# Kernel tuning notes

Measured on AMD Instinct MI355X. Metric: run time of the kernel, lower is better.

The kernel has to match this reference:

```python
import jax, jax.numpy as jnp
import numpy as np

SCALE = 0.125  # 1/sqrt(d_k), d_k = 64


def setup_inputs() -> dict:
    key = jax.random.key(0)
    kq, kk, kv, kp = jax.random.split(key, 4)
    H, B, L, T, D = 16, 4, 1024, 1024, 64
    return {
        "query": jax.random.normal(kq, (H, B, L, D), dtype=jnp.float32),
        "key": jax.random.normal(kk, (H, B, T, D), dtype=jnp.float32),
        "value": jax.random.normal(kv, (H, B, T, D), dtype=jnp.float32),
        "prev_attention": jax.random.normal(kp, (H, B, L, T), dtype=jnp.float32),
    }


def reference(query, key, value, prev_attention):
    # scores: [h, b, l, t]
    scores = jnp.einsum("hblk,hbtk->hblt", query, key) * SCALE
    scores = scores + prev_attention
    attention = jax.nn.softmax(scores, axis=-1)
    # dropout disabled (rate 0.0) for deterministic reference
    output = jnp.einsum("hblt,hbtv->hblv", attention, value)
    return (output, attention)
```

## Files before the change

### kernel.cpp

```cpp
#include <hip/hip_runtime.h>

#define SCALE 0.125f

constexpr int L_ = 1024, T_ = 1024, D_ = 64, HB_ = 64;

using f32x4 = __attribute__((ext_vector_type(4))) float;
using half8 = __attribute__((ext_vector_type(8))) _Float16;
using half4 = __attribute__((ext_vector_type(4))) _Float16;

__global__ __launch_bounds__(256) void cvt_v(const float* __restrict__ v,
                                             _Float16* __restrict__ vh) {
  __shared__ _Float16 ts[64][136];
  const int tid = threadIdx.x;
  const int hb = blockIdx.y;
  const int t0 = blockIdx.x * 128;
  {
    const int tr = tid >> 1, dh = (tid & 1) * 32;
    const float* p = v + ((size_t)hb * T_ + t0 + tr) * D_ + dh;
#pragma unroll
    for (int i = 0; i < 8; ++i) {
      f32x4 r = *(const f32x4*)(p + i * 4);
#pragma unroll
      for (int e = 0; e < 4; ++e) ts[dh + i * 4 + e][tr] = (_Float16)r[e];
    }
  }
  __syncthreads();
  {
    const int d = tid >> 2, tq = (tid & 3) * 32;
    _Float16* qo = vh + ((size_t)hb * D_ + d) * T_ + t0 + tq;
#pragma unroll
    for (int i = 0; i < 4; ++i)
      *(half8*)(qo + i * 8) = *(const half8*)&ts[d][tq + i * 8];
  }
}

__global__ __launch_bounds__(512) void attn_all(
    const float* __restrict__ q, const float* __restrict__ kk,
    const _Float16* __restrict__ Vh, const float* __restrict__ prev,
    float* __restrict__ out, float* __restrict__ att) {
  __shared__ __align__(16) _Float16 Ks[1024][70];
  __shared__ __align__(16) _Float16 Pl[8][16][64];

  const int ltile = blockIdx.x;
  const int hb    = blockIdx.y;
  const int tid = threadIdx.x;
  const int w = tid >> 6, l = tid & 63, l15 = l & 15, lg = l >> 4;
  const int qrow = ltile * 128 + w * 16 + l15;

  auto plb = [&](int row, int byte) -> _Float16* {
    return (_Float16*)((unsigned char*)&Pl[w][0][0] + row * 128 +
                       ((unsigned)byte ^ (((unsigned)row & 7) << 4)));
  };

  {
    const int srow = tid >> 2, scol = (tid & 3) * 16;
    const float* kp0 = kk + (size_t)hb * T_ * D_;
#pragma unroll
    for (int rep = 0; rep < 8; ++rep) {
      const int r = rep * 128 + srow;
      const float* p = kp0 + (size_t)r * D_ + scol;
      f32x4 a = *(const f32x4*)(p);
      f32x4 b = *(const f32x4*)(p + 4);
      f32x4 cc = *(const f32x4*)(p + 8);
      f32x4 d = *(const f32x4*)(p + 12);
      half8 h0, h1;
#pragma unroll
      for (int e = 0; e < 4; ++e) {
        h0[e] = (_Float16)a[e];  h0[4 + e] = (_Float16)b[e];
        h1[e] = (_Float16)cc[e]; h1[4 + e] = (_Float16)d[e];
      }
      *(half8*)&Ks[r][scol] = h0;
      *(half8*)&Ks[r][scol + 8] = h1;
    }
  }

  half8 qb2[2];
  {
    const float* qp = q + ((size_t)hb * L_ + qrow) * D_ + lg * 8;
#pragma unroll
    for (int f = 0; f < 2; ++f)
#pragma unroll
      for (int e = 0; e < 8; ++e) qb2[f][e] = (_Float16)qp[f * 32 + e];
  }

  const float* prowb =
      prev + ((size_t)hb * L_ + ltile * 128 + w * 16) * (size_t)T_;
  const int cr = l >> 4, cc4 = (l & 15) * 4;

  f32x4 pr[2][4];
  auto pload = [&](int c, int s) {
#pragma unroll
    for (int i = 0; i < 4; ++i)
      pr[s][i] =
          *(const f32x4*)(prowb + (size_t)(cr + 4 * i) * T_ + c * 64 + cc4);
  };
  auto pstage = [&](int s) {
#pragma unroll
    for (int i = 0; i < 4; ++i) {
      half4 h;
      h[0] = (_Float16)pr[s][i][0]; h[1] = (_Float16)pr[s][i][1];
      h[2] = (_Float16)pr[s][i][2]; h[3] = (_Float16)pr[s][i][3];
      *(half4*)plb(cr + 4 * i, cc4 * 2) = h;
    }
  };

  __syncthreads();

  pload(0, 0);
  pload(1, 1);
  float zsum = 0.f;

#pragma unroll 2
  for (int c = 0; c < 16; ++c) {
    pstage(c & 1);
    if (c < 14) pload(c + 2, c & 1);

#pragma unroll
    for (int nt = 0; nt < 4; ++nt) {
      const int trow = c * 64 + nt * 16 + l15;
      half8 ka0 = *(const half8*)&Ks[trow][lg * 8];
      half8 ka1 = *(const half8*)&Ks[trow][32 + lg * 8];
      f32x4 acc = {0.f, 0.f, 0.f, 0.f};
      acc = __builtin_amdgcn_mfma_f32_16x16x32_f16(ka0, qb2[0], acc, 0, 0, 0);
      acc = __builtin_amdgcn_mfma_f32_16x16x32_f16(ka1, qb2[1], acc, 0, 0, 0);

      half4 hv = *(const half4*)plb(l15, (nt * 16 + lg * 4) * 2);
      zsum += __expf(acc[0] * SCALE + (float)hv[0]);
      zsum += __expf(acc[1] * SCALE + (float)hv[1]);
      zsum += __expf(acc[2] * SCALE + (float)hv[2]);
      zsum += __expf(acc[3] * SCALE + (float)hv[3]);
    }
  }

  zsum += __shfl_xor(zsum, 16, 64);
  zsum += __shfl_xor(zsum, 32, 64);
  const float rzq = 1.0f / zsum;

  const _Float16* vbh = Vh + (size_t)hb * D_ * T_;
  float* attb = att + ((size_t)hb * L_ + ltile * 128 + w * 16) * (size_t)T_;

  half8 vr[2][8];
  auto vload = [&](int c, int s) {
#pragma unroll
    for (int ks = 0; ks < 2; ++ks)
#pragma unroll
      for (int nd = 0; nd < 4; ++nd)
        vr[s][ks * 4 + nd] =
            *(const half8*)(vbh + (size_t)(nd * 16 + l15) * T_ + c * 64 +
                            ks * 32 + lg * 8);
  };

  pload(0, 0);
  pload(1, 1);
  vload(0, 0);
  vload(1, 1);

  f32x4 oacc[4];
#pragma unroll
  for (int nd = 0; nd < 4; ++nd) oacc[nd] = (f32x4){0.f, 0.f, 0.f, 0.f};

#pragma unroll 2
  for (int c = 0; c < 16; ++c) {
    pstage(c & 1);
    if (c < 14) pload(c + 2, c & 1);

#pragma unroll
    for (int nt = 0; nt < 4; ++nt) {
      const int trow = c * 64 + nt * 16 + l15;
      half8 ka0 = *(const half8*)&Ks[trow][lg * 8];
      half8 ka1 = *(const half8*)&Ks[trow][32 + lg * 8];
      f32x4 acc = {0.f, 0.f, 0.f, 0.f};
      acc = __builtin_amdgcn_mfma_f32_16x16x32_f16(ka0, qb2[0], acc, 0, 0, 0);
      acc = __builtin_amdgcn_mfma_f32_16x16x32_f16(ka1, qb2[1], acc, 0, 0, 0);

      half4 hv = *(const half4*)plb(l15, (nt * 16 + lg * 4) * 2);
      float s0 = __expf(acc[0] * SCALE + (float)hv[0]) * rzq;
      float s1 = __expf(acc[1] * SCALE + (float)hv[1]) * rzq;
      float s2 = __expf(acc[2] * SCALE + (float)hv[2]) * rzq;
      float s3 = __expf(acc[3] * SCALE + (float)hv[3]) * rzq;
      half4 sv;
      sv[0] = (_Float16)s0; sv[1] = (_Float16)s1;
      sv[2] = (_Float16)s2; sv[3] = (_Float16)s3;
      *(half4*)plb(l15, (nt * 16 + lg * 4) * 2) = sv;
    }

#pragma unroll
    for (int ks = 0; ks < 2; ++ks) {
      half8 af = *(const half8*)plb(l15, (ks * 32 + lg * 8) * 2);
#pragma unroll
      for (int nd = 0; nd < 4; ++nd)
        oacc[nd] = __builtin_amdgcn_mfma_f32_16x16x32_f16(
            af, vr[c & 1][ks * 4 + nd], oacc[nd], 0, 0, 0);
    }

#pragma unroll
    for (int i = 0; i < 4; ++i) {
      half4 hv = *(const half4*)plb(cr + 4 * i, cc4 * 2);
      f32x4 sv = {(float)hv[0], (float)hv[1], (float)hv[2], (float)hv[3]};
      *(f32x4*)(attb + (size_t)(cr + 4 * i) * T_ + c * 64 + cc4) = sv;
    }

    if (c < 14) vload(c + 2, c & 1);
  }

  float* outw =
      out + ((size_t)hb * L_ + ltile * 128 + w * 16 + lg * 4) * (size_t)D_;
#pragma unroll
  for (int nd = 0; nd < 4; ++nd)
#pragma unroll
    for (int i = 0; i < 4; ++i)
      outw[(size_t)i * D_ + nd * 16 + l15] = oacc[nd][i];
}

extern "C" void kernel_launch(void* const* d_in, const int* in_sizes, int n_in,
                              void* d_out, int out_size, void* d_ws,
                              size_t ws_size, hipStream_t stream) {
  const float* q    = (const float*)d_in[0];
  const float* k    = (const float*)d_in[1];
  const float* v    = (const float*)d_in[2];
  const float* prev = (const float*)d_in[3];

  float* out = (float*)d_out;
  float* att = out + (size_t)HB_ * L_ * D_;

  _Float16* Vh = (_Float16*)d_ws;

  cvt_v<<<dim3(T_ / 128, HB_), 256, 0, stream>>>(v, Vh);
  attn_all<<<dim3(L_ / 128, HB_), 512, 0, stream>>>(q, k, Vh, prev, out, att);
}
```

Measured before the change: 209.4 us.

## Cache unnormalized exponentials in registers to skip second pass recompute and prev reload

The first softmax pass now keeps every exp(score) as fp16 in a per-thread register array while it accumulates the row sum. The second pass just scales those cached values by the reciprocal sum, so it no longer reloads prev_attention from global memory or recomputes the QK^T MFMAs and exponentials. This cuts the dominant global read traffic roughly in half. In exchange it adds heavy register pressure (128 extra VGPRs, full loop unroll), which risks spills or lower occupancy, and it rounds exp values to fp16 before normalising.

```diff
diff --git a/kernel.cpp b/kernel.cpp
--- a/kernel.cpp
+++ b/kernel.cpp
@@ -106,11 +106,12 @@
 
   __syncthreads();
 
+  half4 E[16][4];
   pload(0, 0);
   pload(1, 1);
   float zsum = 0.f;
 
-#pragma unroll 2
+#pragma unroll
   for (int c = 0; c < 16; ++c) {
     pstage(c & 1);
     if (c < 14) pload(c + 2, c & 1);
@@ -125,16 +126,21 @@
       acc = __builtin_amdgcn_mfma_f32_16x16x32_f16(ka1, qb2[1], acc, 0, 0, 0);
 
       half4 hv = *(const half4*)plb(l15, (nt * 16 + lg * 4) * 2);
-      zsum += __expf(acc[0] * SCALE + (float)hv[0]);
-      zsum += __expf(acc[1] * SCALE + (float)hv[1]);
-      zsum += __expf(acc[2] * SCALE + (float)hv[2]);
-      zsum += __expf(acc[3] * SCALE + (float)hv[3]);
+      float e0 = __expf(acc[0] * SCALE + (float)hv[0]);
+      float e1 = __expf(acc[1] * SCALE + (float)hv[1]);
+      float e2 = __expf(acc[2] * SCALE + (float)hv[2]);
+      float e3 = __expf(acc[3] * SCALE + (float)hv[3]);
+      zsum += (e0 + e1) + (e2 + e3);
+      half4 ev;
+      ev[0] = (_Float16)e0; ev[1] = (_Float16)e1;
+      ev[2] = (_Float16)e2; ev[3] = (_Float16)e3;
+      E[c][nt] = ev;
     }
   }
 
   zsum += __shfl_xor(zsum, 16, 64);
   zsum += __shfl_xor(zsum, 32, 64);
-  const float rzq = 1.0f / zsum;
+  const _Float16 rzh = (_Float16)(1.0f / zsum);
 
   const _Float16* vbh = Vh + (size_t)hb * D_ * T_;
   float* attb = att + ((size_t)hb * L_ + ltile * 128 + w * 16) * (size_t)T_;
@@ -149,9 +155,6 @@
             *(const half8*)(vbh + (size_t)(nd * 16 + l15) * T_ + c * 64 +
                             ks * 32 + lg * 8);
   };
-
-  pload(0, 0);
-  pload(1, 1);
   vload(0, 0);
   vload(1, 1);
 
@@ -159,28 +162,14 @@
 #pragma unroll
   for (int nd = 0; nd < 4; ++nd) oacc[nd] = (f32x4){0.f, 0.f, 0.f, 0.f};
 
-#pragma unroll 2
+#pragma unroll
   for (int c = 0; c < 16; ++c) {
-    pstage(c & 1);
-    if (c < 14) pload(c + 2, c & 1);
-
 #pragma unroll
     for (int nt = 0; nt < 4; ++nt) {
-      const int trow = c * 64 + nt * 16 + l15;
-      half8 ka0 = *(const half8*)&Ks[trow][lg * 8];
-      half8 ka1 = *(const half8*)&Ks[trow][32 + lg * 8];
-      f32x4 acc = {0.f, 0.f, 0.f, 0.f};
-      acc = __builtin_amdgcn_mfma_f32_16x16x32_f16(ka0, qb2[0], acc, 0, 0, 0);
-      acc = __builtin_amdgcn_mfma_f32_16x16x32_f16(ka1, qb2[1], acc, 0, 0, 0);
-
-      half4 hv = *(const half4*)plb(l15, (nt * 16 + lg * 4) * 2);
-      float s0 = __expf(acc[0] * SCALE + (float)hv[0]) * rzq;
-      float s1 = __expf(acc[1] * SCALE + (float)hv[1]) * rzq;
-      float s2 = __expf(acc[2] * SCALE + (float)hv[2]) * rzq;
-      float s3 = __expf(acc[3] * SCALE + (float)hv[3]) * rzq;
+      half4 ev = E[c][nt];
       half4 sv;
-      sv[0] = (_Float16)s0; sv[1] = (_Float16)s1;
-      sv[2] = (_Float16)s2; sv[3] = (_Float16)s3;
+      sv[0] = ev[0] * rzh; sv[1] = ev[1] * rzh;
+      sv[2] = ev[2] * rzh; sv[3] = ev[3] * rzh;
       *(half4*)plb(l15, (nt * 16 + lg * 4) * 2) = sv;
     }
 
@@ -194,10 +183,10 @@
     }
 
 #pragma unroll
-    for (int i = 0; i < 4; ++i) {
-      half4 hv = *(const half4*)plb(cr + 4 * i, cc4 * 2);
+    for (int j = 0; j < 4; ++j) {
+      half4 hv = *(const half4*)plb(cr + 4 * j, cc4 * 2);
       f32x4 sv = {(float)hv[0], (float)hv[1], (float)hv[2], (float)hv[3]};
-      *(f32x4*)(attb + (size_t)(cr + 4 * i) * T_ + c * 64 + cc4) = sv;
+      *(f32x4*)(attb + (size_t)(cr + 4 * j) * T_ + c * 64 + cc4) = sv;
     }
 
     if (c < 14) vload(c + 2, c & 1);
```

Result: slower. 367.7 us (+75.6%).
